# Performance work log

Measured on AMD Instinct MI355X. Metric: run time of the kernel, lower is better.

The kernel has to match this reference:

```python
import jax, jax.numpy as jnp
import numpy as np

N = 50000       # nodes
E = 800000      # edges (avg degree 16)
IN = 256        # input feature dim
HID = 64        # per-head hidden dim
H = 2           # heads
C = 64          # num_classes (final single-head layer width)
NEG_SLOPE = 0.01  # torch F.leaky_relu default


def setup_inputs() -> dict:
    key = jax.random.key(0)
    ks = jax.random.split(key, 24)
    nrm = lambda k, shape, scale: jax.random.normal(k, shape, jnp.float32) * scale
    features = nrm(ks[0], (N, IN), 1.0)
    src = jax.random.randint(ks[1], (E,), 0, N)
    dst = jax.random.randint(ks[2], (E,), 0, N)
    # layer 0: H heads, Linear(IN->HID) + attn_l/attn_r Linear(HID->1)
    W0 = nrm(ks[3], (H, IN, HID), IN ** -0.5)
    b0 = jnp.zeros((H, HID), jnp.float32)
    al0 = nrm(ks[4], (H, HID), HID ** -0.5)
    bl0 = jnp.zeros((H,), jnp.float32)
    ar0 = nrm(ks[5], (H, HID), HID ** -0.5)
    br0 = jnp.zeros((H,), jnp.float32)
    # layer 1: H heads, Linear(H*HID->HID)
    W1 = nrm(ks[6], (H, H * HID, HID), (H * HID) ** -0.5)
    b1 = jnp.zeros((H, HID), jnp.float32)
    al1 = nrm(ks[7], (H, HID), HID ** -0.5)
    bl1 = jnp.zeros((H,), jnp.float32)
    ar1 = nrm(ks[8], (H, HID), HID ** -0.5)
    br1 = jnp.zeros((H,), jnp.float32)
    # final: 1 head, Linear(H*HID->C)
    Wf = nrm(ks[9], (1, H * HID, C), (H * HID) ** -0.5)
    bf = jnp.zeros((1, C), jnp.float32)
    alf = nrm(ks[10], (1, C), C ** -0.5)
    blf = jnp.zeros((1,), jnp.float32)
    arf = nrm(ks[11], (1, C), C ** -0.5)
    brf = jnp.zeros((1,), jnp.float32)
    return dict(features=features, src=src, dst=dst,
                W0=W0, b0=b0, al0=al0, bl0=bl0, ar0=ar0, br0=br0,
                W1=W1, b1=b1, al1=al1, bl1=bl1, ar1=ar1, br1=br1,
                Wf=Wf, bf=bf, alf=alf, blf=blf, arf=arf, brf=brf)


def gat_layer(x, src, dst, W, b, al, bl, ar, br):
    # x: [N, D]; W: [H, D, K]
    ft = jnp.einsum('nd,hdk->nhk', x, W) + b          # [N,H,K]
    a1 = jnp.einsum('nhk,hk->nh', ft, al) + bl        # [N,H] (dst-side)
    a2 = jnp.einsum('nhk,hk->nh', ft, ar) + br        # [N,H] (src-side)
    s = jax.nn.leaky_relu(a1[dst] + a2[src], NEG_SLOPE)  # [E,H]
    m = jax.ops.segment_max(s, dst, num_segments=N)      # per-dst max for stable softmax
    e = jnp.exp(s - m[dst])
    denom = jax.ops.segment_sum(e, dst, num_segments=N)
    alpha = e / denom[dst]                               # edge softmax over in-neighbors
    accum = jax.ops.segment_sum(alpha[:, :, None] * ft[src], dst, num_segments=N)  # [N,H,K]
    return jax.nn.elu(accum)


def reference(features, src, dst,
              W0, b0, al0, bl0, ar0, br0,
              W1, b1, al1, bl1, ar1, br1,
              Wf, bf, alf, blf, arf, brf):
    x = gat_layer(features, src, dst, W0, b0, al0, bl0, ar0, br0).reshape(N, H * HID)
    x = gat_layer(x, src, dst, W1, b1, al1, bl1, ar1, br1).reshape(N, H * HID)
    out = gat_layer(x, src, dst, Wf, bf, alf, blf, arf, brf)[:, 0, :]  # [N,C]
    return out
```

## Files before the change

### kernel.cpp

```cpp
#include <hip/hip_runtime.h>
#include <math.h>

#define NN 50000
#define EE 800000
#define DIN 256
#define NEG_SLOPE 0.01f

typedef __attribute__((ext_vector_type(8))) short bf16x8;
typedef __attribute__((ext_vector_type(8))) unsigned short u16x8;
typedef __attribute__((ext_vector_type(4))) float f32x4;
typedef __attribute__((ext_vector_type(2))) _Float16 f16x2;
typedef __attribute__((ext_vector_type(4))) _Float16 f16x4;

__device__ __forceinline__ unsigned short bf16_rne(float f) {
    unsigned int u = __float_as_uint(f);
    u += 0x7fffu + ((u >> 16) & 1u);
    return (unsigned short)(u >> 16);
}
__device__ __forceinline__ float bf16_tof(unsigned short h) {
    return __uint_as_float(((unsigned int)h) << 16);
}

__global__ __launch_bounds__(256) void histrank_kernel(const int* __restrict__ dst,
                                                       int* __restrict__ cnt,
                                                       int* __restrict__ pos, int E) {
    int e = blockIdx.x * 256 + threadIdx.x;
    if (e < E) pos[e] = atomicAdd(&cnt[dst[e]], 1);
}

__global__ __launch_bounds__(1024) void scanA_kernel(const int* __restrict__ cnt,
                                                     int* __restrict__ off,
                                                     int* __restrict__ aux, int Nn) {
    __shared__ int wsums[16];
    int tid = threadIdx.x, lane = tid & 63, w = tid >> 6;
    int i = blockIdx.x * 1024 + tid;
    int v = (i < Nn) ? cnt[i] : 0;
    int x = v;
#pragma unroll
    for (int d = 1; d < 64; d <<= 1) {
        int y = __shfl_up(x, d);
        if (lane >= d) x += y;
    }
    if (lane == 63) wsums[w] = x;
    __syncthreads();
    if (w == 0 && lane < 16) {
        int ws = wsums[lane];
#pragma unroll
        for (int d = 1; d < 16; d <<= 1) {
            int y = __shfl_up(ws, d);
            if (lane >= d) ws += y;
        }
        wsums[lane] = ws;
    }
    __syncthreads();
    int incl = x + (w > 0 ? wsums[w - 1] : 0);
    if (i < Nn) off[i + 1] = incl;
    if (tid == 1023) aux[blockIdx.x] = incl;
}

__global__ __launch_bounds__(1024) void scanC_kernel(const int* __restrict__ aux,
                                                     int* __restrict__ off, int Nn) {
    int b = blockIdx.x;
    int prefix = 0;
    for (int j = 0; j < b; j++) prefix += aux[j];
    int i = b * 1024 + threadIdx.x;
    if (i < Nn) off[i + 1] += prefix;
    if (i == 0 && b == 0) off[0] = 0;
}

__global__ __launch_bounds__(256) void scatter_kernel(const int* __restrict__ src,
                                                      const int* __restrict__ dst,
                                                      const int* __restrict__ off,
                                                      const int* __restrict__ pos,
                                                      int* __restrict__ esrc, int E) {
    int e = blockIdx.x * 256 + threadIdx.x;
    if (e >= E) return;
    int d = dst[e];
    esrc[off[d] + pos[e]] = src[e];
}

__global__ __launch_bounds__(256) void conv_w_kernel(
    const float* __restrict__ W0, const float* __restrict__ W1,
    const float* __restrict__ Wf, unsigned short* __restrict__ w0h,
    unsigned short* __restrict__ w0l, unsigned short* __restrict__ w1h,
    unsigned short* __restrict__ w1l, unsigned short* __restrict__ wfh,
    unsigned short* __restrict__ wfl) {
    int t = blockIdx.x * 256 + threadIdx.x;
    const float* W;
    unsigned short *oh, *ol;
    int D, u;
    if (t < 32768) { W = W0; oh = w0h; ol = w0l; D = 256; u = t; }
    else if (t < 49152) { W = W1; oh = w1h; ol = w1l; D = 128; u = t - 32768; }
    else if (t < 57344) { W = Wf; oh = wfh; ol = wfl; D = 128; u = t - 49152; }
    else return;
    int d = u & (D - 1);
    int n = u / D;
    float v = W[((size_t)(n >> 6) * D + d) * 64 + (n & 63)];
    unsigned short hi = bf16_rne(v);
    unsigned short lo = bf16_rne(v - bf16_tof(hi));
    oh[(size_t)n * D + d] = hi;
    ol[(size_t)n * D + d] = lo;
}

#define LDK 40

template <int NCOL, bool AFP32>
__global__ __launch_bounds__(256) void gemm_attn(
    const float* __restrict__ Xf, const unsigned short* __restrict__ Xhi,
    const unsigned short* __restrict__ Xlo, const unsigned short* __restrict__ Wthi,
    const unsigned short* __restrict__ Wtlo, const float* __restrict__ bias,
    const float* __restrict__ al, const float* __restrict__ bl,
    const float* __restrict__ ar, const float* __restrict__ br,
    _Float16* __restrict__ FT, float* __restrict__ A1, float* __restrict__ A2,
    int Nn, int D) {
    const int H = NCOL / 64;
    const int NC16 = NCOL / 16;
    __shared__ __align__(16) unsigned short Ahi_s[64 * LDK];
    __shared__ __align__(16) unsigned short Alo_s[64 * LDK];
    __shared__ __align__(16) unsigned short Bhi_s[NCOL * LDK];
    __shared__ __align__(16) unsigned short Blo_s[NCOL * LDK];

    int tid = threadIdx.x;
    int wv = tid >> 6, l = tid & 63, lm = l & 15, quad = l >> 4;
    int m0 = blockIdx.x * 64;

    f32x4 acc[NC16];
#pragma unroll
    for (int c = 0; c < NC16; c++) acc[c] = (f32x4){0.f, 0.f, 0.f, 0.f};

    for (int d0 = 0; d0 < D; d0 += 32) {
        if (AFP32) {
#pragma unroll
            for (int i = 0; i < 2; i++) {
                int u = tid + i * 256;
                int row = u >> 3, c4 = u & 7;
                float4 v = make_float4(0.f, 0.f, 0.f, 0.f);
                if (m0 + row < Nn)
                    v = *(const float4*)&Xf[(size_t)(m0 + row) * D + d0 + c4 * 4];
                float f[4] = {v.x, v.y, v.z, v.w};
                unsigned short hi[4], lo[4];
#pragma unroll
                for (int j = 0; j < 4; j++) {
                    hi[j] = bf16_rne(f[j]);
                    lo[j] = bf16_rne(f[j] - bf16_tof(hi[j]));
                }
                *(ushort4*)&Ahi_s[row * LDK + c4 * 4] = make_ushort4(hi[0], hi[1], hi[2], hi[3]);
                *(ushort4*)&Alo_s[row * LDK + c4 * 4] = make_ushort4(lo[0], lo[1], lo[2], lo[3]);
            }
        } else {
            int row = tid >> 2, q = tid & 3;
            u16x8 vh = (u16x8)0, vl = (u16x8)0;
            if (m0 + row < Nn) {
                vh = *(const u16x8*)&Xhi[(size_t)(m0 + row) * D + d0 + q * 8];
                vl = *(const u16x8*)&Xlo[(size_t)(m0 + row) * D + d0 + q * 8];
            }
            *(u16x8*)&Ahi_s[row * LDK + q * 8] = vh;
            *(u16x8*)&Alo_s[row * LDK + q * 8] = vl;
        }
#pragma unroll
        for (int i = 0; i < NCOL / 64; i++) {
            int u = tid + i * 256;
            int n = u >> 2, q = u & 3;
            *(u16x8*)&Bhi_s[n * LDK + q * 8] =
                *(const u16x8*)&Wthi[(size_t)n * D + d0 + q * 8];
            *(u16x8*)&Blo_s[n * LDK + q * 8] =
                *(const u16x8*)&Wtlo[(size_t)n * D + d0 + q * 8];
        }
        __syncthreads();

        int arow = wv * 16 + lm;
        bf16x8 ah = *(const bf16x8*)&Ahi_s[arow * LDK + quad * 8];
        bf16x8 alo = *(const bf16x8*)&Alo_s[arow * LDK + quad * 8];
#pragma unroll
        for (int c = 0; c < NC16; c++) {
            bf16x8 bh = *(const bf16x8*)&Bhi_s[(c * 16 + lm) * LDK + quad * 8];
            bf16x8 blo = *(const bf16x8*)&Blo_s[(c * 16 + lm) * LDK + quad * 8];
            acc[c] = __builtin_amdgcn_mfma_f32_16x16x32_bf16(ah, bh, acc[c], 0, 0, 0);
            acc[c] = __builtin_amdgcn_mfma_f32_16x16x32_bf16(ah, blo, acc[c], 0, 0, 0);
            acc[c] = __builtin_amdgcn_mfma_f32_16x16x32_bf16(alo, bh, acc[c], 0, 0, 0);
        }
        __syncthreads();
    }

    float bj[NC16], alj[NC16], arj[NC16];
#pragma unroll
    for (int c = 0; c < NC16; c++) {
        bj[c] = bias[c * 16 + lm];
        alj[c] = al[c * 16 + lm];
        arj[c] = ar[c * 16 + lm];
    }
#pragma unroll
    for (int reg = 0; reg < 4; reg++) {
        int row = m0 + wv * 16 + quad * 4 + reg;
        bool ok = row < Nn;
        float s1[H], s2[H];
#pragma unroll
        for (int h = 0; h < H; h++) { s1[h] = 0.f; s2[h] = 0.f; }
#pragma unroll
        for (int c = 0; c < NC16; c++) {
            float o = acc[c][reg] + bj[c];
            int h = c >> 2;
            s1[h] += o * alj[c];
            s2[h] += o * arj[c];
            if (ok) FT[(size_t)row * NCOL + c * 16 + lm] = (_Float16)o;
        }
#pragma unroll
        for (int h = 0; h < H; h++) {
#pragma unroll
            for (int d = 1; d < 16; d <<= 1) {
                s1[h] += __shfl_xor(s1[h], d);
                s2[h] += __shfl_xor(s2[h], d);
            }
        }
        if (ok && lm == 0) {
#pragma unroll
            for (int h = 0; h < H; h++) {
                A1[(size_t)row * H + h] = s1[h] + bl[h];
                A2[(size_t)row * H + h] = s2[h] + br[h];
            }
        }
    }
}

__global__ __launch_bounds__(256) void agg2_kernel(
    const _Float16* __restrict__ ft, const float* __restrict__ a1,
    const float* __restrict__ a2, const int* __restrict__ off,
    const int* __restrict__ esrc, unsigned short* __restrict__ ohi,
    unsigned short* __restrict__ olo, int Nn) {
    __shared__ __align__(16) float ws[4][128];
    __shared__ __align__(16) int sjs[4][64];
    int wv = threadIdx.x >> 6, lane = threadIdx.x & 63;
    int n = blockIdx.x * 4 + wv;
    if (n >= Nn) return;
    int o0 = off[n], deg = off[n + 1] - o0;
    int g = lane >> 5;
    int el = (lane & 31) * 4;
    int h = (lane & 31) >> 4;
    if (deg == 0) {
        if (g == 0) {
            *(ushort4*)&ohi[(size_t)n * 128 + el] = make_ushort4(0, 0, 0, 0);
            *(ushort4*)&olo[(size_t)n * 128 + el] = make_ushort4(0, 0, 0, 0);
        }
        return;
    }
    float2 a1v = *(const float2*)&a1[(size_t)n * 2];
    float ac0 = 0.f, ac1 = 0.f, ac2 = 0.f, ac3 = 0.f;
    float ds0 = 0.f, ds1 = 0.f;
    for (int e0 = 0; e0 < deg; e0 += 64) {
        int nE = min(64, deg - e0);
        float w0 = 0.f, w1 = 0.f;
        int sj = 0;
        if (lane < nE) {
            sj = esrc[o0 + e0 + lane];
            float2 a2j = *(const float2*)&a2[(size_t)sj * 2];
            float t0 = a1v.x + a2j.x;
            float t1 = a1v.y + a2j.y;
            t0 = t0 > 0.f ? t0 : NEG_SLOPE * t0;
            t1 = t1 > 0.f ? t1 : NEG_SLOPE * t1;
            w0 = __expf(t0);
            w1 = __expf(t1);
        }
        ds0 += w0;
        ds1 += w1;
        *(float2*)&ws[wv][lane * 2] = make_float2(w0, w1);
        sjs[wv][lane] = sj;
        int npair = (nE + 1) >> 1;
        int p = 0;
        for (; p + 8 <= npair; p += 8) {
            float wb[8];
            int sb[8];
#pragma unroll
            for (int u = 0; u < 8; u++) {
                int e = (p + u) * 2 + g;
                wb[u] = ws[wv][e * 2 + h];
                sb[u] = sjs[wv][e];
            }
            f16x4 f[8];
#pragma unroll
            for (int u = 0; u < 8; u++)
                f[u] = *(const f16x4*)&ft[(size_t)sb[u] * 128 + el];
#pragma unroll
            for (int u = 0; u < 8; u++) {
                ac0 += wb[u] * (float)f[u].x;
                ac1 += wb[u] * (float)f[u].y;
                ac2 += wb[u] * (float)f[u].z;
                ac3 += wb[u] * (float)f[u].w;
            }
        }
        for (; p < npair; p++) {
            int e = p * 2 + g;
            float w = ws[wv][e * 2 + h];
            int s0 = sjs[wv][e];
            f16x4 f = *(const f16x4*)&ft[(size_t)s0 * 128 + el];
            ac0 += w * (float)f.x;
            ac1 += w * (float)f.y;
            ac2 += w * (float)f.z;
            ac3 += w * (float)f.w;
        }
    }
    ac0 += __shfl_xor(ac0, 32);
    ac1 += __shfl_xor(ac1, 32);
    ac2 += __shfl_xor(ac2, 32);
    ac3 += __shfl_xor(ac3, 32);
#pragma unroll
    for (int d = 1; d < 64; d <<= 1) {
        ds0 += __shfl_xor(ds0, d);
        ds1 += __shfl_xor(ds1, d);
    }
    if (g == 0) {
        float rd = 1.f / (h ? ds1 : ds0);
        float r[4] = {ac0 * rd, ac1 * rd, ac2 * rd, ac3 * rd};
        unsigned short rh[4], rl[4];
#pragma unroll
        for (int u = 0; u < 4; u++) {
            float v = r[u] > 0.f ? r[u] : expm1f(r[u]);
            rh[u] = bf16_rne(v);
            rl[u] = bf16_rne(v - bf16_tof(rh[u]));
        }
        *(ushort4*)&ohi[(size_t)n * 128 + el] = make_ushort4(rh[0], rh[1], rh[2], rh[3]);
        *(ushort4*)&olo[(size_t)n * 128 + el] = make_ushort4(rl[0], rl[1], rl[2], rl[3]);
    }
}

__global__ __launch_bounds__(256) void agg1_kernel(
    const _Float16* __restrict__ ft, const float* __restrict__ a1,
    const float* __restrict__ a2, const int* __restrict__ off,
    const int* __restrict__ esrc, float* __restrict__ out, int Nn) {
    __shared__ __align__(16) float ws[4][64];
    __shared__ __align__(16) int sjs[4][64];
    int wv = threadIdx.x >> 6, lane = threadIdx.x & 63;
    int n = blockIdx.x * 4 + wv;
    if (n >= Nn) return;
    int o0 = off[n], deg = off[n + 1] - o0;
    int g = lane >> 4;
    int el = (lane & 15) * 4;
    if (deg == 0) {
        if (g == 0) *(float4*)&out[(size_t)n * 64 + el] = make_float4(0.f, 0.f, 0.f, 0.f);
        return;
    }
    float a1v = a1[n];
    float ac0 = 0.f, ac1 = 0.f, ac2 = 0.f, ac3 = 0.f;
    float dsum = 0.f;
    for (int e0 = 0; e0 < deg; e0 += 64) {
        int nE = min(64, deg - e0);
        float wl = 0.f;
        int sj = 0;
        if (lane < nE) {
            sj = esrc[o0 + e0 + lane];
            float t = a1v + a2[sj];
            t = t > 0.f ? t : NEG_SLOPE * t;
            wl = __expf(t);
        }
        dsum += wl;
        ws[wv][lane] = wl;
        sjs[wv][lane] = sj;
        int nquad = (nE + 3) >> 2;
        int q = 0;
        for (; q + 4 <= nquad; q += 4) {
            float wb[4];
            int sb[4];
#pragma unroll
            for (int u = 0; u < 4; u++) {
                int e = (q + u) * 4 + g;
                wb[u] = ws[wv][e];
                sb[u] = sjs[wv][e];
            }
            f16x4 f[4];
#pragma unroll
            for (int u = 0; u < 4; u++)
                f[u] = *(const f16x4*)&ft[(size_t)sb[u] * 64 + el];
#pragma unroll
            for (int u = 0; u < 4; u++) {
                ac0 += wb[u] * (float)f[u].x;
                ac1 += wb[u] * (float)f[u].y;
                ac2 += wb[u] * (float)f[u].z;
                ac3 += wb[u] * (float)f[u].w;
            }
        }
        for (; q < nquad; q++) {
            int e = q * 4 + g;
            float w = ws[wv][e];
            int s0 = sjs[wv][e];
            f16x4 f = *(const f16x4*)&ft[(size_t)s0 * 64 + el];
            ac0 += w * (float)f.x;
            ac1 += w * (float)f.y;
            ac2 += w * (float)f.z;
            ac3 += w * (float)f.w;
        }
    }
    ac0 += __shfl_xor(ac0, 16);
    ac1 += __shfl_xor(ac1, 16);
    ac2 += __shfl_xor(ac2, 16);
    ac3 += __shfl_xor(ac3, 16);
    ac0 += __shfl_xor(ac0, 32);
    ac1 += __shfl_xor(ac1, 32);
    ac2 += __shfl_xor(ac2, 32);
    ac3 += __shfl_xor(ac3, 32);
#pragma unroll
    for (int d = 1; d < 64; d <<= 1) dsum += __shfl_xor(dsum, d);
    if (g == 0) {
        float rd = 1.f / dsum;
        float r[4] = {ac0 * rd, ac1 * rd, ac2 * rd, ac3 * rd};
#pragma unroll
        for (int u = 0; u < 4; u++) r[u] = r[u] > 0.f ? r[u] : expm1f(r[u]);
        *(float4*)&out[(size_t)n * 64 + el] = make_float4(r[0], r[1], r[2], r[3]);
    }
}

extern "C" void kernel_launch(void* const* d_in, const int* in_sizes, int n_in,
                              void* d_out, int out_size, void* d_ws, size_t ws_size,
                              hipStream_t stream) {
    const float* features = (const float*)d_in[0];
    const int* src = (const int*)d_in[1];
    const int* dst = (const int*)d_in[2];
    const float* W0 = (const float*)d_in[3];
    const float* b0 = (const float*)d_in[4];
    const float* al0 = (const float*)d_in[5];
    const float* bl0 = (const float*)d_in[6];
    const float* ar0 = (const float*)d_in[7];
    const float* br0 = (const float*)d_in[8];
    const float* W1 = (const float*)d_in[9];
    const float* b1 = (const float*)d_in[10];
    const float* al1 = (const float*)d_in[11];
    const float* bl1 = (const float*)d_in[12];
    const float* ar1 = (const float*)d_in[13];
    const float* br1 = (const float*)d_in[14];
    const float* Wf = (const float*)d_in[15];
    const float* bf = (const float*)d_in[16];
    const float* alf = (const float*)d_in[17];
    const float* blf = (const float*)d_in[18];
    const float* arf = (const float*)d_in[19];
    const float* brf = (const float*)d_in[20];

    char* p = (char*)d_ws;
    auto carve = [&](size_t bytes) {
        void* q = (void*)p;
        p += (bytes + 255) & ~(size_t)255;
        return q;
    };
    _Float16* ft = (_Float16*)carve((size_t)NN * 128 * 2);
    unsigned short* Xhi = (unsigned short*)carve((size_t)NN * 128 * 2);
    unsigned short* Xlo = (unsigned short*)carve((size_t)NN * 128 * 2);
    float* a1 = (float*)carve((size_t)NN * 2 * 4);
    float* a2 = (float*)carve((size_t)NN * 2 * 4);
    int* off = (int*)carve((size_t)(NN + 1) * 4);
    int* cnt = (int*)carve((size_t)NN * 4);
    int* esrc = (int*)carve((size_t)EE * 4);
    int* pos = (int*)carve((size_t)EE * 4);
    int* aux = (int*)carve(64 * 4);
    unsigned short* w0h = (unsigned short*)carve(32768 * 2);
    unsigned short* w0l = (unsigned short*)carve(32768 * 2);
    unsigned short* w1h = (unsigned short*)carve(16384 * 2);
    unsigned short* w1l = (unsigned short*)carve(16384 * 2);
    unsigned short* wfh = (unsigned short*)carve(8192 * 2);
    unsigned short* wfl = (unsigned short*)carve(8192 * 2);

    const int NB_SCAN = (NN + 1023) / 1024;
    const int GE = (EE + 255) / 256;

    hipMemsetAsync(cnt, 0, (size_t)NN * 4, stream);
    histrank_kernel<<<GE, 256, 0, stream>>>(dst, cnt, pos, EE);
    scanA_kernel<<<NB_SCAN, 1024, 0, stream>>>(cnt, off, aux, NN);
    scanC_kernel<<<NB_SCAN, 1024, 0, stream>>>(aux, off, NN);
    scatter_kernel<<<GE, 256, 0, stream>>>(src, dst, off, pos, esrc, EE);
    conv_w_kernel<<<(57344 + 255) / 256, 256, 0, stream>>>(W0, W1, Wf, w0h, w0l, w1h,
                                                           w1l, wfh, wfl);

    const int gx = (NN + 63) / 64;
    const int gn = (NN + 3) / 4;

    gemm_attn<128, true><<<gx, 256, 0, stream>>>(features, nullptr, nullptr, w0h, w0l,
                                                 b0, al0, bl0, ar0, br0, ft, a1, a2,
                                                 NN, DIN);
    agg2_kernel<<<gn, 256, 0, stream>>>(ft, a1, a2, off, esrc, Xhi, Xlo, NN);

    gemm_attn<128, false><<<gx, 256, 0, stream>>>(nullptr, Xhi, Xlo, w1h, w1l, b1, al1,
                                                  bl1, ar1, br1, ft, a1, a2, NN, 128);
    agg2_kernel<<<gn, 256, 0, stream>>>(ft, a1, a2, off, esrc, Xhi, Xlo, NN);

    gemm_attn<64, false><<<gx, 256, 0, stream>>>(nullptr, Xhi, Xlo, wfh, wfl, bf, alf,
                                                 blf, arf, brf, ft, a1, a2, NN, 128);
    agg1_kernel<<<gn, 256, 0, stream>>>(ft, a1, a2, off, esrc, (float*)d_out, NN);
}
```

Measured before the change: 348.6 us.

## Split GAT aggregation into edge-weight pass and column-sliced gather pass

Each fused aggregation kernel becomes two kernels. The first computes per-edge softmax numerators packed with the source index and stores per-node reciprocal denominators. The second gathers features with four (or two) blocks per node, each owning a 32-column slice, which gives more parallelism and shorter per-lane gather rows. The cost is extra global traffic for the packed (src, weight) arrays, a second read of them by every column slice, and twice as many kernel launches.

```diff
diff --git a/kernel.cpp b/kernel.cpp
--- a/kernel.cpp
+++ b/kernel.cpp
@@ -9,7 +9,6 @@
 typedef __attribute__((ext_vector_type(8))) short bf16x8;
 typedef __attribute__((ext_vector_type(8))) unsigned short u16x8;
 typedef __attribute__((ext_vector_type(4))) float f32x4;
-typedef __attribute__((ext_vector_type(2))) _Float16 f16x2;
 typedef __attribute__((ext_vector_type(4))) _Float16 f16x4;
 
 __device__ __forceinline__ unsigned short bf16_rne(float f) {
@@ -222,172 +221,127 @@
     }
 }
 
-__global__ __launch_bounds__(256) void agg2_kernel(
-    const _Float16* __restrict__ ft, const float* __restrict__ a1,
-    const float* __restrict__ a2, const int* __restrict__ off,
-    const int* __restrict__ esrc, unsigned short* __restrict__ ohi,
-    unsigned short* __restrict__ olo, int Nn) {
-    __shared__ __align__(16) float ws[4][128];
-    __shared__ __align__(16) int sjs[4][64];
+__global__ __launch_bounds__(256) void wgt2_kernel(
+    const float* __restrict__ a1, const float* __restrict__ a2,
+    const int* __restrict__ off, const int* __restrict__ esrc,
+    int2* __restrict__ pk0, int2* __restrict__ pk1, float* __restrict__ rd,
+    int Nn) {
     int wv = threadIdx.x >> 6, lane = threadIdx.x & 63;
     int n = blockIdx.x * 4 + wv;
     if (n >= Nn) return;
     int o0 = off[n], deg = off[n + 1] - o0;
-    int g = lane >> 5;
-    int el = (lane & 31) * 4;
-    int h = (lane & 31) >> 4;
-    if (deg == 0) {
-        if (g == 0) {
-            *(ushort4*)&ohi[(size_t)n * 128 + el] = make_ushort4(0, 0, 0, 0);
-            *(ushort4*)&olo[(size_t)n * 128 + el] = make_ushort4(0, 0, 0, 0);
-        }
-        return;
-    }
+    if (deg == 0) return;
     float2 a1v = *(const float2*)&a1[(size_t)n * 2];
-    float ac0 = 0.f, ac1 = 0.f, ac2 = 0.f, ac3 = 0.f;
     float ds0 = 0.f, ds1 = 0.f;
     for (int e0 = 0; e0 < deg; e0 += 64) {
-        int nE = min(64, deg - e0);
-        float w0 = 0.f, w1 = 0.f;
-        int sj = 0;
-        if (lane < nE) {
-            sj = esrc[o0 + e0 + lane];
+        if (e0 + lane < deg) {
+            int sj = esrc[o0 + e0 + lane];
             float2 a2j = *(const float2*)&a2[(size_t)sj * 2];
             float t0 = a1v.x + a2j.x;
             float t1 = a1v.y + a2j.y;
             t0 = t0 > 0.f ? t0 : NEG_SLOPE * t0;
             t1 = t1 > 0.f ? t1 : NEG_SLOPE * t1;
-            w0 = __expf(t0);
-            w1 = __expf(t1);
-        }
-        ds0 += w0;
-        ds1 += w1;
-        *(float2*)&ws[wv][lane * 2] = make_float2(w0, w1);
-        sjs[wv][lane] = sj;
-        int npair = (nE + 1) >> 1;
-        int p = 0;
-        for (; p + 8 <= npair; p += 8) {
-            float wb[8];
-            int sb[8];
-#pragma unroll
-            for (int u = 0; u < 8; u++) {
-                int e = (p + u) * 2 + g;
-                wb[u] = ws[wv][e * 2 + h];
-                sb[u] = sjs[wv][e];
-            }
-            f16x4 f[8];
-#pragma unroll
-            for (int u = 0; u < 8; u++)
-                f[u] = *(const f16x4*)&ft[(size_t)sb[u] * 128 + el];
-#pragma unroll
-            for (int u = 0; u < 8; u++) {
-                ac0 += wb[u] * (float)f[u].x;
-                ac1 += wb[u] * (float)f[u].y;
-                ac2 += wb[u] * (float)f[u].z;
-                ac3 += wb[u] * (float)f[u].w;
-            }
-        }
-        for (; p < npair; p++) {
-            int e = p * 2 + g;
-            float w = ws[wv][e * 2 + h];
-            int s0 = sjs[wv][e];
-            f16x4 f = *(const f16x4*)&ft[(size_t)s0 * 128 + el];
-            ac0 += w * (float)f.x;
-            ac1 += w * (float)f.y;
-            ac2 += w * (float)f.z;
-            ac3 += w * (float)f.w;
-        }
-    }
-    ac0 += __shfl_xor(ac0, 32);
-    ac1 += __shfl_xor(ac1, 32);
-    ac2 += __shfl_xor(ac2, 32);
-    ac3 += __shfl_xor(ac3, 32);
+            float w0 = __expf(t0);
+            float w1 = __expf(t1);
+            ds0 += w0;
+            ds1 += w1;
+            pk0[o0 + e0 + lane] = make_int2(sj, __float_as_int(w0));
+            pk1[o0 + e0 + lane] = make_int2(sj, __float_as_int(w1));
+        }
+    }
 #pragma unroll
     for (int d = 1; d < 64; d <<= 1) {
         ds0 += __shfl_xor(ds0, d);
         ds1 += __shfl_xor(ds1, d);
     }
-    if (g == 0) {
-        float rd = 1.f / (h ? ds1 : ds0);
-        float r[4] = {ac0 * rd, ac1 * rd, ac2 * rd, ac3 * rd};
-        unsigned short rh[4], rl[4];
-#pragma unroll
-        for (int u = 0; u < 4; u++) {
-            float v = r[u] > 0.f ? r[u] : expm1f(r[u]);
-            rh[u] = bf16_rne(v);
-            rl[u] = bf16_rne(v - bf16_tof(rh[u]));
-        }
-        *(ushort4*)&ohi[(size_t)n * 128 + el] = make_ushort4(rh[0], rh[1], rh[2], rh[3]);
-        *(ushort4*)&olo[(size_t)n * 128 + el] = make_ushort4(rl[0], rl[1], rl[2], rl[3]);
-    }
-}
-
-__global__ __launch_bounds__(256) void agg1_kernel(
-    const _Float16* __restrict__ ft, const float* __restrict__ a1,
-    const float* __restrict__ a2, const int* __restrict__ off,
-    const int* __restrict__ esrc, float* __restrict__ out, int Nn) {
-    __shared__ __align__(16) float ws[4][64];
-    __shared__ __align__(16) int sjs[4][64];
+    if (lane == 0) *(float2*)&rd[(size_t)n * 2] = make_float2(1.f / ds0, 1.f / ds1);
+}
+
+__global__ __launch_bounds__(256) void wgtf_kernel(
+    const float* __restrict__ a1, const float* __restrict__ a2,
+    const int* __restrict__ off, const int* __restrict__ esrc,
+    int2* __restrict__ pk, float* __restrict__ rd, int Nn) {
     int wv = threadIdx.x >> 6, lane = threadIdx.x & 63;
     int n = blockIdx.x * 4 + wv;
     if (n >= Nn) return;
     int o0 = off[n], deg = off[n + 1] - o0;
-    int g = lane >> 4;
-    int el = (lane & 15) * 4;
+    if (deg == 0) return;
+    float a1v = a1[n];
+    float ds = 0.f;
+    for (int e0 = 0; e0 < deg; e0 += 64) {
+        if (e0 + lane < deg) {
+            int sj = esrc[o0 + e0 + lane];
+            float t = a1v + a2[sj];
+            t = t > 0.f ? t : NEG_SLOPE * t;
+            float w = __expf(t);
+            ds += w;
+            pk[o0 + e0 + lane] = make_int2(sj, __float_as_int(w));
+        }
+    }
+#pragma unroll
+    for (int d = 1; d < 64; d <<= 1) ds += __shfl_xor(ds, d);
+    if (lane == 0) rd[n] = 1.f / ds;
+}
+
+__global__ __launch_bounds__(256) void sagg2_kernel(
+    const _Float16* __restrict__ ft, const int2* __restrict__ pk0,
+    const int2* __restrict__ pk1, const float* __restrict__ rd,
+    const int* __restrict__ off, unsigned short* __restrict__ ohi,
+    unsigned short* __restrict__ olo, int Nn) {
+    __shared__ __align__(16) int2 pks[4][64];
+    int wv = threadIdx.x >> 6, lane = threadIdx.x & 63;
+    int s = blockIdx.x & 3;
+    int n = (blockIdx.x >> 2) * 4 + wv;
+    if (n >= Nn) return;
+    int g = lane >> 3;
+    int el = (lane & 7) * 4;
+    int col = s * 32 + el;
+    int o0 = off[n], deg = off[n + 1] - o0;
     if (deg == 0) {
-        if (g == 0) *(float4*)&out[(size_t)n * 64 + el] = make_float4(0.f, 0.f, 0.f, 0.f);
+        if (lane < 8) {
+            *(ushort4*)&ohi[(size_t)n * 128 + col] = make_ushort4(0, 0, 0, 0);
+            *(ushort4*)&olo[(size_t)n * 128 + col] = make_ushort4(0, 0, 0, 0);
+        }
         return;
     }
-    float a1v = a1[n];
+    const int2* __restrict__ pk = (s >> 1) ? pk1 : pk0;
     float ac0 = 0.f, ac1 = 0.f, ac2 = 0.f, ac3 = 0.f;
-    float dsum = 0.f;
     for (int e0 = 0; e0 < deg; e0 += 64) {
         int nE = min(64, deg - e0);
-        float wl = 0.f;
-        int sj = 0;
-        if (lane < nE) {
-            sj = esrc[o0 + e0 + lane];
-            float t = a1v + a2[sj];
-            t = t > 0.f ? t : NEG_SLOPE * t;
-            wl = __expf(t);
-        }
-        dsum += wl;
-        ws[wv][lane] = wl;
-        sjs[wv][lane] = sj;
-        int nquad = (nE + 3) >> 2;
+        int2 p = make_int2(0, 0);
+        if (lane < nE) p = pk[o0 + e0 + lane];
+        pks[wv][lane] = p;
+        int noct = (nE + 7) >> 3;
         int q = 0;
-        for (; q + 4 <= nquad; q += 4) {
-            float wb[4];
-            int sb[4];
-#pragma unroll
-            for (int u = 0; u < 4; u++) {
-                int e = (q + u) * 4 + g;
-                wb[u] = ws[wv][e];
-                sb[u] = sjs[wv][e];
-            }
-            f16x4 f[4];
-#pragma unroll
-            for (int u = 0; u < 4; u++)
-                f[u] = *(const f16x4*)&ft[(size_t)sb[u] * 64 + el];
-#pragma unroll
-            for (int u = 0; u < 4; u++) {
-                ac0 += wb[u] * (float)f[u].x;
-                ac1 += wb[u] * (float)f[u].y;
-                ac2 += wb[u] * (float)f[u].z;
-                ac3 += wb[u] * (float)f[u].w;
-            }
-        }
-        for (; q < nquad; q++) {
-            int e = q * 4 + g;
-            float w = ws[wv][e];
-            int s0 = sjs[wv][e];
-            f16x4 f = *(const f16x4*)&ft[(size_t)s0 * 64 + el];
-            ac0 += w * (float)f.x;
-            ac1 += w * (float)f.y;
-            ac2 += w * (float)f.z;
-            ac3 += w * (float)f.w;
-        }
-    }
+        for (; q + 2 <= noct; q += 2) {
+            int2 pa = pks[wv][q * 8 + g];
+            int2 pb = pks[wv][q * 8 + 8 + g];
+            f16x4 fa = *(const f16x4*)&ft[(size_t)pa.x * 128 + col];
+            f16x4 fb = *(const f16x4*)&ft[(size_t)pb.x * 128 + col];
+            float wa = __int_as_float(pa.y), wb = __int_as_float(pb.y);
+            ac0 += wa * (float)fa.x;
+            ac1 += wa * (float)fa.y;
+            ac2 += wa * (float)fa.z;
+            ac3 += wa * (float)fa.w;
+            ac0 += wb * (float)fb.x;
+            ac1 += wb * (float)fb.y;
+            ac2 += wb * (float)fb.z;
+            ac3 += wb * (float)fb.w;
+        }
+        for (; q < noct; q++) {
+            int2 pa = pks[wv][q * 8 + g];
+            f16x4 fa = *(const f16x4*)&ft[(size_t)pa.x * 128 + col];
+            float wa = __int_as_float(pa.y);
+            ac0 += wa * (float)fa.x;
+            ac1 += wa * (float)fa.y;
+            ac2 += wa * (float)fa.z;
+            ac3 += wa * (float)fa.w;
+        }
+    }
+    ac0 += __shfl_xor(ac0, 8);
+    ac1 += __shfl_xor(ac1, 8);
+    ac2 += __shfl_xor(ac2, 8);
+    ac3 += __shfl_xor(ac3, 8);
     ac0 += __shfl_xor(ac0, 16);
     ac1 += __shfl_xor(ac1, 16);
     ac2 += __shfl_xor(ac2, 16);
@@ -396,14 +350,89 @@
     ac1 += __shfl_xor(ac1, 32);
     ac2 += __shfl_xor(ac2, 32);
     ac3 += __shfl_xor(ac3, 32);
-#pragma unroll
-    for (int d = 1; d < 64; d <<= 1) dsum += __shfl_xor(dsum, d);
-    if (g == 0) {
-        float rd = 1.f / dsum;
-        float r[4] = {ac0 * rd, ac1 * rd, ac2 * rd, ac3 * rd};
+    if (lane < 8) {
+        float rdv = rd[(size_t)n * 2 + (s >> 1)];
+        float r[4] = {ac0 * rdv, ac1 * rdv, ac2 * rdv, ac3 * rdv};
+        unsigned short rh[4], rl[4];
+#pragma unroll
+        for (int u = 0; u < 4; u++) {
+            float v = r[u] > 0.f ? r[u] : expm1f(r[u]);
+            rh[u] = bf16_rne(v);
+            rl[u] = bf16_rne(v - bf16_tof(rh[u]));
+        }
+        *(ushort4*)&ohi[(size_t)n * 128 + col] = make_ushort4(rh[0], rh[1], rh[2], rh[3]);
+        *(ushort4*)&olo[(size_t)n * 128 + col] = make_ushort4(rl[0], rl[1], rl[2], rl[3]);
+    }
+}
+
+__global__ __launch_bounds__(256) void saggf_kernel(
+    const _Float16* __restrict__ ft, const int2* __restrict__ pk,
+    const float* __restrict__ rd, const int* __restrict__ off,
+    float* __restrict__ out, int Nn) {
+    __shared__ __align__(16) int2 pks[4][64];
+    int wv = threadIdx.x >> 6, lane = threadIdx.x & 63;
+    int s = blockIdx.x & 1;
+    int n = (blockIdx.x >> 1) * 4 + wv;
+    if (n >= Nn) return;
+    int g = lane >> 3;
+    int el = (lane & 7) * 4;
+    int col = s * 32 + el;
+    int o0 = off[n], deg = off[n + 1] - o0;
+    if (deg == 0) {
+        if (lane < 8) *(float4*)&out[(size_t)n * 64 + col] = make_float4(0.f, 0.f, 0.f, 0.f);
+        return;
+    }
+    float ac0 = 0.f, ac1 = 0.f, ac2 = 0.f, ac3 = 0.f;
+    for (int e0 = 0; e0 < deg; e0 += 64) {
+        int nE = min(64, deg - e0);
+        int2 p = make_int2(0, 0);
+        if (lane < nE) p = pk[o0 + e0 + lane];
+        pks[wv][lane] = p;
+        int noct = (nE + 7) >> 3;
+        int q = 0;
+        for (; q + 2 <= noct; q += 2) {
+            int2 pa = pks[wv][q * 8 + g];
+            int2 pb = pks[wv][q * 8 + 8 + g];
+            f16x4 fa = *(const f16x4*)&ft[(size_t)pa.x * 64 + col];
+            f16x4 fb = *(const f16x4*)&ft[(size_t)pb.x * 64 + col];
+            float wa = __int_as_float(pa.y), wb = __int_as_float(pb.y);
+            ac0 += wa * (float)fa.x;
+            ac1 += wa * (float)fa.y;
+            ac2 += wa * (float)fa.z;
+            ac3 += wa * (float)fa.w;
+            ac0 += wb * (float)fb.x;
+            ac1 += wb * (float)fb.y;
+            ac2 += wb * (float)fb.z;
+            ac3 += wb * (float)fb.w;
+        }
+        for (; q < noct; q++) {
+            int2 pa = pks[wv][q * 8 + g];
+            f16x4 fa = *(const f16x4*)&ft[(size_t)pa.x * 64 + col];
+            float wa = __int_as_float(pa.y);
+            ac0 += wa * (float)fa.x;
+            ac1 += wa * (float)fa.y;
+            ac2 += wa * (float)fa.z;
+            ac3 += wa * (float)fa.w;
+        }
+    }
+    ac0 += __shfl_xor(ac0, 8);
+    ac1 += __shfl_xor(ac1, 8);
+    ac2 += __shfl_xor(ac2, 8);
+    ac3 += __shfl_xor(ac3, 8);
+    ac0 += __shfl_xor(ac0, 16);
+    ac1 += __shfl_xor(ac1, 16);
+    ac2 += __shfl_xor(ac2, 16);
+    ac3 += __shfl_xor(ac3, 16);
+    ac0 += __shfl_xor(ac0, 32);
+    ac1 += __shfl_xor(ac1, 32);
+    ac2 += __shfl_xor(ac2, 32);
+    ac3 += __shfl_xor(ac3, 32);
+    if (lane < 8) {
+        float rdv = rd[n];
+        float r[4] = {ac0 * rdv, ac1 * rdv, ac2 * rdv, ac3 * rdv};
 #pragma unroll
         for (int u = 0; u < 4; u++) r[u] = r[u] > 0.f ? r[u] : expm1f(r[u]);
-        *(float4*)&out[(size_t)n * 64 + el] = make_float4(r[0], r[1], r[2], r[3]);
+        *(float4*)&out[(size_t)n * 64 + col] = make_float4(r[0], r[1], r[2], r[3]);
     }
 }
 
@@ -443,10 +472,13 @@
     unsigned short* Xlo = (unsigned short*)carve((size_t)NN * 128 * 2);
     float* a1 = (float*)carve((size_t)NN * 2 * 4);
     float* a2 = (float*)carve((size_t)NN * 2 * 4);
+    float* rd = (float*)carve((size_t)NN * 2 * 4);
     int* off = (int*)carve((size_t)(NN + 1) * 4);
     int* cnt = (int*)carve((size_t)NN * 4);
     int* esrc = (int*)carve((size_t)EE * 4);
     int* pos = (int*)carve((size_t)EE * 4);
+    int2* pk0 = (int2*)carve((size_t)EE * 8);
+    int2* pk1 = (int2*)carve((size_t)EE * 8);
     int* aux = (int*)carve(64 * 4);
     unsigned short* w0h = (unsigned short*)carve(32768 * 2);
     unsigned short* w0l = (unsigned short*)carve(32768 * 2);
@@ -472,13 +504,16 @@
     gemm_attn<128, true><<<gx, 256, 0, stream>>>(features, nullptr, nullptr, w0h, w0l,
                                                  b0, al0, bl0, ar0, br0, ft, a1, a2,
                                                  NN, DIN);
-    agg2_kernel<<<gn, 256, 0, stream>>>(ft, a1, a2, off, esrc, Xhi, Xlo, NN);
+    wgt2_kernel<<<gn, 256, 0, stream>>>(a1, a2, off, esrc, pk0, pk1, rd, NN);
+    sagg2_kernel<<<gn * 4, 256, 0, stream>>>(ft, pk0, pk1, rd, off, Xhi, Xlo, NN);
 
     gemm_attn<128, false><<<gx, 256, 0, stream>>>(nullptr, Xhi, Xlo, w1h, w1l, b1, al1,
                                                   bl1, ar1, br1, ft, a1, a2, NN, 128);
-    agg2_kernel<<<gn, 256, 0, stream>>>(ft, a1, a2, off, esrc, Xhi, Xlo, NN);
+    wgt2_kernel<<<gn, 256, 0, stream>>>(a1, a2, off, esrc, pk0, pk1, rd, NN);
+    sagg2_kernel<<<gn * 4, 256, 0, stream>>>(ft, pk0, pk1, rd, off, Xhi, Xlo, NN);
 
     gemm_attn<64, false><<<gx, 256, 0, stream>>>(nullptr, Xhi, Xlo, wfh, wfl, bf, alf,
                                                  blf, arf, brf, ft, a1, a2, NN, 128);
-    agg1_kernel<<<gn, 256, 0, stream>>>(ft, a1, a2, off, esrc, (float*)d_out, NN);
-}
+    wgtf_kernel<<<gn, 256, 0, stream>>>(a1, a2, off, esrc, pk0, rd, NN);
+    saggf_kernel<<<gn * 2, 256, 0, stream>>>(ft, pk0, rd, off, (float*)d_out, NN);
+}
```

New measurement: 489.5 us. 1.4x slower.
